# Kernel optimization log

Hardware: AMD Instinct MI355X
Metric: run time of the kernel (lower is better)

The kernel has to match this reference:

```python
import jax, jax.numpy as jnp
import numpy as np

N_NODES = 100000
N_EDGES = 1600000
D_FEAT = 64


def setup_inputs() -> dict:
    key = jax.random.key(0)
    k1, k2, k3, k4 = jax.random.split(key, 4)
    row = jnp.sort(jax.random.randint(k1, (N_EDGES,), 0, N_NODES, dtype=jnp.int32))
    col = jax.random.randint(k2, (N_EDGES,), 0, N_NODES, dtype=jnp.int32)
    values = jax.random.uniform(k3, (N_EDGES,), dtype=jnp.float32)
    x = jax.random.normal(k4, (N_NODES, D_FEAT), dtype=jnp.float32)
    return {"row": row, "col": col, "values": values, "x": x}


def reference(row, col, values, x):
    # spmm_scatter: out[row[e]] += values[e] * x[col[e]]  (gather-multiply-scatter)
    msgs = x[col] * values[:, None]                      # [E, d]
    out = jax.ops.segment_sum(msgs, row, num_segments=x.shape[0])  # [N, d]
    return out
```

## Files before the change

### kernel.cpp

```cpp
#include <hip/hip_runtime.h>


constexpr int D  = 64;
constexpr int DV = D / 4;

__global__ __launch_bounds__(256) void spmm_psearch(
    const int* __restrict__ row,
    const int* __restrict__ col,
    const float* __restrict__ val,
    const float4* __restrict__ x4,
    float4* __restrict__ out4,
    int nEdges, int nNodes)
{
    const int wid = (blockIdx.x * blockDim.x + threadIdx.x) >> 6;
    if (wid >= nNodes) return;
    const int lane  = threadIdx.x & 63;
    const int group = lane >> 4;
    const int sub   = lane & 15;

    int lo = 0, hi = nEdges;
    const int t0 = wid;
    while (hi > lo) {
        const int span = hi - lo + 1;
        if (span <= 64) {
            const int idx = lo + lane;
            const bool lt = (idx <= hi) && (idx < nEdges) && (row[idx] < t0);
            lo += __popcll(__ballot(lt));
            break;
        }
        const int step = (span + 63) >> 6;
        const int idx  = lo + lane * step;
        const bool lt  = (idx <= hi) && (idx < nEdges) && (row[idx] < t0);
        const int  c   = __popcll(__ballot(lt));
        if (c == 0) { hi = lo; break; }
        const int new_lo = lo + (c - 1) * step + 1;
        if (c < 64) hi = lo + c * step;
        lo = new_lo;
    }
    const int start = lo;

    const int t1 = wid + 1;
    int end = start;
    for (;;) {
        const int idx = end + lane;
        const bool lt = (idx < nEdges) && (row[idx] < t1);
        const int  c  = __popcll(__ballot(lt));
        end += c;
        if (c < 64) break;
    }

    float4 acc = {0.f, 0.f, 0.f, 0.f};
    for (int e = start + group; e < end; e += 16) {
        const int e1 = e + 4, e2 = e + 8, e3 = e + 12;
        const int   c0 = col[e];
        const float v0 = val[e];
        int c1 = c0, c2 = c0, c3 = c0;
        float v1 = 0.f, v2 = 0.f, v3 = 0.f;
        if (e1 < end) { c1 = col[e1]; v1 = val[e1]; }
        if (e2 < end) { c2 = col[e2]; v2 = val[e2]; }
        if (e3 < end) { c3 = col[e3]; v3 = val[e3]; }
        const float4 x0 = x4[(size_t)c0 * DV + sub];
        const float4 x1 = x4[(size_t)c1 * DV + sub];
        const float4 x2 = x4[(size_t)c2 * DV + sub];
        const float4 x3 = x4[(size_t)c3 * DV + sub];
        acc.x = fmaf(v0, x0.x, acc.x); acc.y = fmaf(v0, x0.y, acc.y);
        acc.z = fmaf(v0, x0.z, acc.z); acc.w = fmaf(v0, x0.w, acc.w);
        acc.x = fmaf(v1, x1.x, acc.x); acc.y = fmaf(v1, x1.y, acc.y);
        acc.z = fmaf(v1, x1.z, acc.z); acc.w = fmaf(v1, x1.w, acc.w);
        acc.x = fmaf(v2, x2.x, acc.x); acc.y = fmaf(v2, x2.y, acc.y);
        acc.z = fmaf(v2, x2.z, acc.z); acc.w = fmaf(v2, x2.w, acc.w);
        acc.x = fmaf(v3, x3.x, acc.x); acc.y = fmaf(v3, x3.y, acc.y);
        acc.z = fmaf(v3, x3.z, acc.z); acc.w = fmaf(v3, x3.w, acc.w);
    }

    #pragma unroll
    for (int off = 16; off <= 32; off <<= 1) {
        acc.x += __shfl_xor(acc.x, off, 64);
        acc.y += __shfl_xor(acc.y, off, 64);
        acc.z += __shfl_xor(acc.z, off, 64);
        acc.w += __shfl_xor(acc.w, off, 64);
    }
    if (group == 0) out4[(size_t)wid * DV + sub] = acc;
}

extern "C" void kernel_launch(void* const* d_in, const int* in_sizes, int n_in,
                              void* d_out, int out_size, void* d_ws, size_t ws_size,
                              hipStream_t stream)
{
    const int*    row  = (const int*)   d_in[0];
    const int*    col  = (const int*)   d_in[1];
    const float*  val  = (const float*) d_in[2];
    const float4* x4   = (const float4*)d_in[3];
    float4*       out4 = (float4*)d_out;

    const int nEdges = in_sizes[0];
    const int nNodes = out_size / D;

    const dim3 block(256);
    const dim3 grid(((size_t)nNodes * 64 + 255) / 256);
    spmm_psearch<<<grid, block, 0, stream>>>(row, col, val, x4, out4, nEdges, nNodes);
}
```

Before: 153.7 us.

## Convert x to fp16 and switch to edge-parallel LDS segmented reduction

Result: slower. 194.1 us (+26.3%).

```diff
diff --git a/kernel.cpp b/kernel.cpp
--- a/kernel.cpp
+++ b/kernel.cpp
@@ -1,8 +1,130 @@
 #include <hip/hip_runtime.h>
-
-
-constexpr int D  = 64;
-constexpr int DV = D / 4;
+#include <hip/hip_fp16.h>
+
+
+constexpr int D       = 64;
+constexpr int DV      = 16;
+constexpr int DH8     = 8;
+constexpr int EPB     = 256;
+constexpr int MAXSPAN = 96;
+
+struct __align__(16) h8 { __half2 a, b, c, d; };
+
+__global__ __launch_bounds__(256) void prep_kernel(
+    const float4* __restrict__ x4,
+    h8* __restrict__ xh,
+    float4* __restrict__ out4,
+    int n8, int nOut4)
+{
+    const int i = blockIdx.x * blockDim.x + threadIdx.x;
+    if (i < nOut4) out4[i] = float4{0.f, 0.f, 0.f, 0.f};
+    if (i < n8) {
+        const float4 lo = x4[2 * i];
+        const float4 hi = x4[2 * i + 1];
+        h8 h;
+        h.a = __float22half2_rn(make_float2(lo.x, lo.y));
+        h.b = __float22half2_rn(make_float2(lo.z, lo.w));
+        h.c = __float22half2_rn(make_float2(hi.x, hi.y));
+        h.d = __float22half2_rn(make_float2(hi.z, hi.w));
+        xh[i] = h;
+    }
+}
+
+__global__ __launch_bounds__(256) void spmm_edge_lds(
+    const int* __restrict__ row,
+    const int* __restrict__ col,
+    const float* __restrict__ val,
+    const h8* __restrict__ xh,
+    float* __restrict__ out,
+    int nEdges, int nNodes)
+{
+    __shared__ __align__(16) float lds[MAXSPAN * D];
+    const int tid  = threadIdx.x;
+    const int lane = tid & 63;
+    const int wg   = tid >> 6;
+    const int sub  = lane & 7;
+    const int base = lane & 56;
+    const int BPE  = blockIdx.x * EPB;
+    const int lastE = nEdges - 1;
+
+    const int r0   = row[min(BPE, lastE)];
+    const int rEnd = row[min(BPE + EPB - 1, lastE)];
+    const int span = rEnd - r0 + 1;
+
+    const int  eL = BPE + wg * 64 + lane;
+    const bool ok = eL < nEdges;
+    const int   rr = row[min(eL, lastE)];
+    const int   cc = ok ? col[eL] : 0;
+    const float vv = ok ? val[eL] : 0.f;
+
+    if (span <= MAXSPAN) {
+        for (int i = tid; i < span * D; i += EPB) lds[i] = 0.f;
+        __syncthreads();
+
+        int cj[8];
+        #pragma unroll
+        for (int j = 0; j < 8; ++j) cj[j] = __shfl(cc, base + j, 64);
+        h8 p[8];
+        #pragma unroll
+        for (int j = 0; j < 8; ++j) p[j] = xh[(size_t)cj[j] * DH8 + sub];
+
+        float acc[8] = {0.f,0.f,0.f,0.f,0.f,0.f,0.f,0.f};
+        int rprev = __shfl(rr, base, 64);
+        #pragma unroll
+        for (int j = 0; j < 8; ++j) {
+            const int   rj = __shfl(rr, base + j, 64);
+            const float vj = __shfl(vv, base + j, 64);
+            if (rj != rprev) {
+                float* dst = &lds[(rprev - r0) * D + sub * 8];
+                #pragma unroll
+                for (int k = 0; k < 8; ++k) { atomicAdd(&dst[k], acc[k]); acc[k] = 0.f; }
+                rprev = rj;
+            }
+            float2 f;
+            f = __half22float2(p[j].a); acc[0] = fmaf(vj, f.x, acc[0]); acc[1] = fmaf(vj, f.y, acc[1]);
+            f = __half22float2(p[j].b); acc[2] = fmaf(vj, f.x, acc[2]); acc[3] = fmaf(vj, f.y, acc[3]);
+            f = __half22float2(p[j].c); acc[4] = fmaf(vj, f.x, acc[4]); acc[5] = fmaf(vj, f.y, acc[5]);
+            f = __half22float2(p[j].d); acc[6] = fmaf(vj, f.x, acc[6]); acc[7] = fmaf(vj, f.y, acc[7]);
+        }
+        {
+            float* dst = &lds[(rprev - r0) * D + sub * 8];
+            #pragma unroll
+            for (int k = 0; k < 8; ++k) atomicAdd(&dst[k], acc[k]);
+        }
+        __syncthreads();
+
+        for (int idx = tid; idx < span * DV; idx += EPB) {
+            const int li = idx >> 4, ch = idx & 15;
+            const int node = r0 + li;
+            const float4 w = *(const float4*)&lds[li * D + ch * 4];
+            float* dst = &out[(size_t)node * D + ch * 4];
+            if (li == 0 || li == span - 1) {
+                atomicAdd(&dst[0], w.x); atomicAdd(&dst[1], w.y);
+                atomicAdd(&dst[2], w.z); atomicAdd(&dst[3], w.w);
+            } else {
+                *(float4*)dst = w;
+            }
+        }
+    } else {
+        #pragma unroll
+        for (int j = 0; j < 8; ++j) {
+            const int   c  = __shfl(cc, base + j, 64);
+            const int   rj = __shfl(rr, base + j, 64);
+            const float vj = __shfl(vv, base + j, 64);
+            const h8 pp = xh[(size_t)c * DH8 + sub];
+            if (vj != 0.f) {
+                float2 f; float t[8];
+                f = __half22float2(pp.a); t[0] = vj * f.x; t[1] = vj * f.y;
+                f = __half22float2(pp.b); t[2] = vj * f.x; t[3] = vj * f.y;
+                f = __half22float2(pp.c); t[4] = vj * f.x; t[5] = vj * f.y;
+                f = __half22float2(pp.d); t[6] = vj * f.x; t[7] = vj * f.y;
+                float* dst = &out[(size_t)rj * D + sub * 8];
+                #pragma unroll
+                for (int k = 0; k < 8; ++k) atomicAdd(&dst[k], t[k]);
+            }
+        }
+    }
+}
 
 __global__ __launch_bounds__(256) void spmm_psearch(
     const int* __restrict__ row,
@@ -38,7 +160,6 @@
         lo = new_lo;
     }
     const int start = lo;
-
     const int t1 = wid + 1;
     int end = start;
     for (;;) {
@@ -50,29 +171,19 @@
     }
 
     float4 acc = {0.f, 0.f, 0.f, 0.f};
-    for (int e = start + group; e < end; e += 16) {
-        const int e1 = e + 4, e2 = e + 8, e3 = e + 12;
+    for (int e = start + group; e < end; e += 8) {
+        const int e1 = e + 4;
         const int   c0 = col[e];
         const float v0 = val[e];
-        int c1 = c0, c2 = c0, c3 = c0;
-        float v1 = 0.f, v2 = 0.f, v3 = 0.f;
+        int c1 = c0; float v1 = 0.f;
         if (e1 < end) { c1 = col[e1]; v1 = val[e1]; }
-        if (e2 < end) { c2 = col[e2]; v2 = val[e2]; }
-        if (e3 < end) { c3 = col[e3]; v3 = val[e3]; }
         const float4 x0 = x4[(size_t)c0 * DV + sub];
         const float4 x1 = x4[(size_t)c1 * DV + sub];
-        const float4 x2 = x4[(size_t)c2 * DV + sub];
-        const float4 x3 = x4[(size_t)c3 * DV + sub];
         acc.x = fmaf(v0, x0.x, acc.x); acc.y = fmaf(v0, x0.y, acc.y);
         acc.z = fmaf(v0, x0.z, acc.z); acc.w = fmaf(v0, x0.w, acc.w);
         acc.x = fmaf(v1, x1.x, acc.x); acc.y = fmaf(v1, x1.y, acc.y);
         acc.z = fmaf(v1, x1.z, acc.z); acc.w = fmaf(v1, x1.w, acc.w);
-        acc.x = fmaf(v2, x2.x, acc.x); acc.y = fmaf(v2, x2.y, acc.y);
-        acc.z = fmaf(v2, x2.z, acc.z); acc.w = fmaf(v2, x2.w, acc.w);
-        acc.x = fmaf(v3, x3.x, acc.x); acc.y = fmaf(v3, x3.y, acc.y);
-        acc.z = fmaf(v3, x3.z, acc.z); acc.w = fmaf(v3, x3.w, acc.w);
-    }
-
+    }
     #pragma unroll
     for (int off = 16; off <= 32; off <<= 1) {
         acc.x += __shfl_xor(acc.x, off, 64);
@@ -91,12 +202,24 @@
     const int*    col  = (const int*)   d_in[1];
     const float*  val  = (const float*) d_in[2];
     const float4* x4   = (const float4*)d_in[3];
-    float4*       out4 = (float4*)d_out;
 
     const int nEdges = in_sizes[0];
     const int nNodes = out_size / D;
+    const int n8     = nNodes * DH8;
+    const int nOut4  = nNodes * DV;
 
     const dim3 block(256);
-    const dim3 grid(((size_t)nNodes * 64 + 255) / 256);
-    spmm_psearch<<<grid, block, 0, stream>>>(row, col, val, x4, out4, nEdges, nNodes);
-}
+    const size_t need = (size_t)nNodes * D * sizeof(__half);
+
+    if (ws_size >= need) {
+        h8* xh = (h8*)d_ws;
+        const int prep_n = (nOut4 > n8) ? nOut4 : n8;
+        prep_kernel<<<dim3((prep_n + 255) / 256), block, 0, stream>>>(
+            x4, xh, (float4*)d_out, n8, nOut4);
+        spmm_edge_lds<<<dim3((nEdges + EPB - 1) / EPB), block, 0, stream>>>(
+            row, col, val, xh, (float*)d_out, nEdges, nNodes);
+    } else {
+        spmm_psearch<<<dim3(((size_t)nNodes * 64 + 255) / 256), block, 0, stream>>>(
+            row, col, val, x4, (float4*)d_out, nEdges, nNodes);
+    }
+}
```
